# Optimization experiments

Hardware: AMD Instinct MI355X
Metric: run time of the kernel (lower is better)

## Reference

```python
import jax, jax.numpy as jnp
import numpy as np
import math

B, S, D = 4, 1024, 1024
NH, HD = 16, 64
I = 4096
EPS = 1e-12


def layer_norm(x, g, b):
    mu = jnp.mean(x, axis=-1, keepdims=True)
    var = jnp.mean((x - mu) ** 2, axis=-1, keepdims=True)
    return (x - mu) * jax.lax.rsqrt(var + EPS) * g + b


def setup_inputs() -> dict:
    key = jax.random.key(0)
    ks = jax.random.split(key, 12)
    s = 0.02
    return {
        "hidden_states": jax.random.normal(ks[0], (B, S, D), jnp.float32),
        "attention_mask": jnp.zeros((B, 1, 1, S), jnp.float32),
        "Wq": jax.random.normal(ks[1], (D, D), jnp.float32) * s,
        "bq": jnp.zeros((D,), jnp.float32),
        "Wk": jax.random.normal(ks[2], (D, D), jnp.float32) * s,
        "bk": jnp.zeros((D,), jnp.float32),
        "Wv": jax.random.normal(ks[3], (D, D), jnp.float32) * s,
        "bv": jnp.zeros((D,), jnp.float32),
        "Wo": jax.random.normal(ks[4], (D, D), jnp.float32) * s,
        "bo": jnp.zeros((D,), jnp.float32),
        "ln1_g": jnp.ones((D,), jnp.float32),
        "ln1_b": jnp.zeros((D,), jnp.float32),
        "Wi": jax.random.normal(ks[5], (D, I), jnp.float32) * s,
        "bi": jnp.zeros((I,), jnp.float32),
        "Wout": jax.random.normal(ks[6], (I, D), jnp.float32) * s,
        "bout": jnp.zeros((D,), jnp.float32),
        "ln2_g": jnp.ones((D,), jnp.float32),
        "ln2_b": jnp.zeros((D,), jnp.float32),
    }


def reference(hidden_states, attention_mask, Wq, bq, Wk, bk, Wv, bv, Wo, bo,
              ln1_g, ln1_b, Wi, bi, Wout, bout, ln2_g, ln2_b):
    h = hidden_states
    # QKV projections, split into heads: [B,S,D] -> [B,NH,S,HD]
    def heads(x):
        return x.reshape(B, S, NH, HD).transpose(0, 2, 1, 3)
    q = heads(h @ Wq + bq)
    k = heads(h @ Wk + bk)
    v = heads(h @ Wv + bv)
    # manual attention: scores [B,NH,S,S]
    scores = jnp.einsum("bhqd,bhkd->bhqk", q, k) / math.sqrt(HD)
    scores = scores + attention_mask
    probs = jax.nn.softmax(scores, axis=-1)
    ctx = jnp.einsum("bhqk,bhkd->bhqd", probs, v)
    ctx = ctx.transpose(0, 2, 1, 3).reshape(B, S, D)
    # self-output: dense + residual + LN
    attn_out = layer_norm(ctx @ Wo + bo + h, ln1_g, ln1_b)
    # FFN: dense + exact gelu, dense + residual + LN
    inter = jax.nn.gelu(attn_out @ Wi + bi, approximate=False)
    out = layer_norm(inter @ Wout + bout + attn_out, ln2_g, ln2_b)
    return out
```

## Files before the change

### kernel.cpp

```cpp
#include <hip/hip_runtime.h>
#include <hip/hip_bf16.h>
#include <math.h>

#define B_ 4
#define S_ 1024
#define D_ 1024
#define NH_ 16
#define HD_ 64
#define I_ 4096
#define M_ (B_*S_)

typedef __bf16 bf16_8 __attribute__((ext_vector_type(8)));
typedef float f32x4 __attribute__((ext_vector_type(4)));
typedef unsigned int u32x2 __attribute__((ext_vector_type(2)));
typedef unsigned short u16;

struct P4 { float* p[4]; };
struct T4 { const float* s[4]; u16* d[4]; };

__device__ __forceinline__ u16 f2b(float x) {
    __hip_bfloat16 h = __float2bfloat16(x);
    return *reinterpret_cast<u16*>(&h);
}

__device__ __forceinline__ void gload16(const void* g, void* l) {
    __builtin_amdgcn_global_load_lds(
        (const __attribute__((address_space(1))) void*)g,
        (__attribute__((address_space(3))) void*)l, 16, 0, 0);
}

__global__ __launch_bounds__(256) void cvt_bf16(
    const float4* __restrict__ in, ushort4* __restrict__ out, int n4)
{
    int i = blockIdx.x * 256 + threadIdx.x;
    if (i < n4) {
        float4 v = in[i];
        ushort4 o;
        o.x = f2b(v.x); o.y = f2b(v.y); o.z = f2b(v.z); o.w = f2b(v.w);
        out[i] = o;
    }
}

__global__ __launch_bounds__(256) void transpose_cvt(
    const float* __restrict__ in, u16* __restrict__ out, int K, int N)
{
    __shared__ float t[32][33];
    const int tid = threadIdx.x;
    const int k0 = blockIdx.y * 32, n0 = blockIdx.x * 32;
#pragma unroll
    for (int i = 0; i < 4; ++i) {
        int idx = i * 256 + tid;
        int r = idx >> 5, c = idx & 31;
        t[r][c] = in[(size_t)(k0 + r) * N + n0 + c];
    }
    __syncthreads();
    const int rr = tid >> 3, cc0 = (tid & 7) * 4;
    ushort4 o;
    o.x = f2b(t[cc0 + 0][rr]);
    o.y = f2b(t[cc0 + 1][rr]);
    o.z = f2b(t[cc0 + 2][rr]);
    o.w = f2b(t[cc0 + 3][rr]);
    *(ushort4*)(out + (size_t)(n0 + rr) * K + k0 + cc0) = o;
}

__global__ __launch_bounds__(256) void transpose4_cvt(T4 t4)
{
    __shared__ float t[32][33];
    const int tid = threadIdx.x;
    const int k0 = blockIdx.y * 32, n0 = blockIdx.x * 32;
    const float* in = t4.s[blockIdx.z];
    u16* out = t4.d[blockIdx.z];
#pragma unroll
    for (int i = 0; i < 4; ++i) {
        int idx = i * 256 + tid;
        int r = idx >> 5, c = idx & 31;
        t[r][c] = in[(size_t)(k0 + r) * D_ + n0 + c];
    }
    __syncthreads();
    const int rr = tid >> 3, cc0 = (tid & 7) * 4;
    ushort4 o;
    o.x = f2b(t[cc0 + 0][rr]);
    o.y = f2b(t[cc0 + 1][rr]);
    o.z = f2b(t[cc0 + 2][rr]);
    o.w = f2b(t[cc0 + 3][rr]);
    *(ushort4*)(out + (size_t)(n0 + rr) * D_ + k0 + cc0) = o;
}

#define NT_ 16

template<int MODE>
__global__ __launch_bounds__(512, 2) void gemm256(
    const u16* __restrict__ A, const u16* __restrict__ Bt,
    const float* __restrict__ b0, const float* __restrict__ b1,
    const float* __restrict__ b2,
    u16* __restrict__ outB, P4 parts, int N, int sA, int sB)
{
    __shared__ __align__(16) char sm[131072];

    const int tid  = threadIdx.x;
    const int lane = tid & 63, wid = tid >> 6;
    const int l15  = lane & 15, lg = lane >> 4;
    const int gm   = wid >> 2, gn = wid & 3;
    const int bm   = blockIdx.y * 256, bn = blockIdx.x * 256;
    const int koff = blockIdx.z * 1024;

    const int srow = (wid << 3) + (lane >> 3);
    const int skb  = ((lane & 7) << 4) ^ (((lane >> 3) & 7) << 4);
    const int scol = skb >> 1;
    const int xm   = (l15 & 7) << 4;

    f32x4 acc[8][4];
#pragma unroll
    for (int m = 0; m < 8; ++m)
#pragma unroll
        for (int j = 0; j < 4; ++j) {
            acc[m][j][0] = 0.f; acc[m][j][1] = 0.f;
            acc[m][j][2] = 0.f; acc[m][j][3] = 0.f;
        }

    auto stageA = [&](int v, int h) {
        const u16* src = A + (size_t)(bm + h * 128 + srow) * sA + koff + v * 64 + scol;
        char* dst = sm + ((v & 1) * 65536 + h * 16384 + wid * 1024);
        gload16(src, dst);
        gload16(src + (size_t)64 * sA, dst + 8192);
    };
    auto stageB = [&](int v, int h) {
        const u16* src = Bt + (size_t)(bn + h * 128 + srow) * sB + koff + v * 64 + scol;
        char* dst = sm + ((v & 1) * 65536 + 32768 + h * 16384 + wid * 1024);
        gload16(src, dst);
        gload16(src + (size_t)64 * sB, dst + 8192);
    };

    bf16_8 a[8], bb[2];
    auto loadA = [&](int vb, int s) {
        const char* base = sm + (vb * 65536 + gm * 16384);
#pragma unroll
        for (int m = 0; m < 8; ++m)
            a[m] = *(const bf16_8*)(base + (m * 16 + l15) * 128 +
                                    ((s * 64 + lg * 16) ^ xm));
    };
    auto loadB = [&](int vb, int s, int np) {
        const char* base = sm + (vb * 65536 + 32768 + (gn >> 1) * 16384);
#pragma unroll
        for (int j = 0; j < 2; ++j)
            bb[j] = *(const bf16_8*)(base + ((gn & 1) * 64 + (np * 2 + j) * 16 + l15) * 128 +
                                     ((s * 64 + lg * 16) ^ xm));
    };
    auto mfma16 = [&](int np) {
#pragma unroll
        for (int m = 0; m < 8; ++m)
#pragma unroll
            for (int j = 0; j < 2; ++j)
                acc[m][np * 2 + j] = __builtin_amdgcn_mfma_f32_16x16x32_bf16(
                    a[m], bb[j], acc[m][np * 2 + j], 0, 0, 0);
    };

    stageA(0, 0); stageA(0, 1);
    stageB(0, 0); stageB(0, 1);
    stageA(1, 0); stageA(1, 1);
    asm volatile("s_waitcnt vmcnt(4)" ::: "memory");
    __builtin_amdgcn_sched_barrier(0);
    __builtin_amdgcn_s_barrier();

    for (int v = 0; v < NT_ - 2; ++v) {
        const int vb = v & 1;
        loadA(vb, 0); loadB(vb, 0, 0);
        stageB(v + 1, 0); stageB(v + 1, 1);
        __builtin_amdgcn_s_barrier();
        asm volatile("s_waitcnt lgkmcnt(0)" ::: "memory");
        __builtin_amdgcn_s_setprio(1); mfma16(0); __builtin_amdgcn_s_setprio(0);
        __builtin_amdgcn_s_barrier();
        loadB(vb, 0, 1);
        __builtin_amdgcn_s_barrier();
        asm volatile("s_waitcnt lgkmcnt(0)" ::: "memory");
        __builtin_amdgcn_s_setprio(1); mfma16(1); __builtin_amdgcn_s_setprio(0);
        __builtin_amdgcn_s_barrier();
        loadA(vb, 1); loadB(vb, 1, 0);
        __builtin_amdgcn_s_barrier();
        asm volatile("s_waitcnt lgkmcnt(0)" ::: "memory");
        __builtin_amdgcn_s_setprio(1); mfma16(0); __builtin_amdgcn_s_setprio(0);
        __builtin_amdgcn_s_barrier();
        loadB(vb, 1, 1);
        stageA(v + 2, 0); stageA(v + 2, 1);
        __builtin_amdgcn_s_barrier();
        asm volatile("s_waitcnt lgkmcnt(0)" ::: "memory");
        __builtin_amdgcn_s_setprio(1); mfma16(1); __builtin_amdgcn_s_setprio(0);
        asm volatile("s_waitcnt vmcnt(4)" ::: "memory");
        __builtin_amdgcn_sched_barrier(0);
        __builtin_amdgcn_s_barrier();
    }
    {
        const int vb = (NT_ - 2) & 1;
        loadA(vb, 0); loadB(vb, 0, 0);
        stageB(NT_ - 1, 0); stageB(NT_ - 1, 1);
        __builtin_amdgcn_s_barrier();
        asm volatile("s_waitcnt lgkmcnt(0)" ::: "memory");
        __builtin_amdgcn_s_setprio(1); mfma16(0); __builtin_amdgcn_s_setprio(0);
        __builtin_amdgcn_s_barrier();
        loadB(vb, 0, 1);
        __builtin_amdgcn_s_barrier();
        asm volatile("s_waitcnt lgkmcnt(0)" ::: "memory");
        __builtin_amdgcn_s_setprio(1); mfma16(1); __builtin_amdgcn_s_setprio(0);
        __builtin_amdgcn_s_barrier();
        loadA(vb, 1); loadB(vb, 1, 0);
        __builtin_amdgcn_s_barrier();
        asm volatile("s_waitcnt lgkmcnt(0)" ::: "memory");
        __builtin_amdgcn_s_setprio(1); mfma16(0); __builtin_amdgcn_s_setprio(0);
        __builtin_amdgcn_s_barrier();
        loadB(vb, 1, 1);
        __builtin_amdgcn_s_barrier();
        asm volatile("s_waitcnt lgkmcnt(0)" ::: "memory");
        __builtin_amdgcn_s_setprio(1); mfma16(1); __builtin_amdgcn_s_setprio(0);
        asm volatile("s_waitcnt vmcnt(0)" ::: "memory");
        __builtin_amdgcn_sched_barrier(0);
        __builtin_amdgcn_s_barrier();
    }
    {
        const int vb = (NT_ - 1) & 1;
        loadA(vb, 0); loadB(vb, 0, 0); mfma16(0);
        loadB(vb, 0, 1);               mfma16(1);
        loadA(vb, 1); loadB(vb, 1, 0); mfma16(0);
        loadB(vb, 1, 1);               mfma16(1);
    }

    if (MODE == 2) {
        float* oP = parts.p[blockIdx.z];
#pragma unroll
        for (int m = 0; m < 8; ++m)
#pragma unroll
            for (int r = 0; r < 4; ++r) {
                const int row = bm + gm * 128 + m * 16 + lg * 4 + r;
#pragma unroll
                for (int j = 0; j < 4; ++j)
                    oP[(size_t)row * N + bn + gn * 64 + j * 16 + l15] = acc[m][j][r];
            }
    } else {
        const int cg = (bn + gn * 64) >> 10;
        const float* bp = (MODE == 0) ? (cg == 0 ? b0 : cg == 1 ? b1 : b2) : b0;
        const int cbase = (MODE == 0) ? ((bn + gn * 64) & 1023) : (bn + gn * 64);
        float bs[4];
#pragma unroll
        for (int j = 0; j < 4; ++j) bs[j] = bp[cbase + j * 16 + l15];
#pragma unroll
        for (int m = 0; m < 8; ++m)
#pragma unroll
            for (int r = 0; r < 4; ++r) {
                const int row = bm + gm * 128 + m * 16 + lg * 4 + r;
#pragma unroll
                for (int j = 0; j < 4; ++j) {
                    float v = acc[m][j][r] + bs[j];
                    if (MODE == 1) {
                        const float u = v * (1.5957691216f + 0.0713548163f * v * v);
                        v = __fdividef(v, 1.0f + __expf(-u));
                    }
                    outB[(size_t)row * N + bn + gn * 64 + j * 16 + l15] = f2b(v);
                }
            }
    }
}

__global__ __launch_bounds__(256) void gemm_splitk(
    const u16* __restrict__ A, const u16* __restrict__ Bt,
    P4 parts, int N, int K, int kchunk)
{
    __shared__ __align__(16) u16 As[128 * 32];
    __shared__ __align__(16) u16 Bs[128 * 32];

    const int tid  = threadIdx.x;
    const int lane = tid & 63, wid = tid >> 6;
    const int l15  = lane & 15, lg = lane >> 4;
    const int wm   = (wid >> 1) * 64, wn = (wid & 1) * 64;
    const int bm   = blockIdx.y * 128, bn = blockIdx.x * 128;
    const int wbase16 = (tid & ~63) * 16;
    const int kt0 = blockIdx.z * kchunk, kt1 = kt0 + kchunk;
    float* outP = parts.p[blockIdx.z];

    const int r0 = tid >> 2;
    const int c0 = (tid & 3) * 8;

    f32x4 acc[4][4];
#pragma unroll
    for (int i = 0; i < 4; ++i)
#pragma unroll
        for (int j = 0; j < 4; ++j) {
            acc[i][j][0] = 0.f; acc[i][j][1] = 0.f;
            acc[i][j][2] = 0.f; acc[i][j][3] = 0.f;
        }

    for (int kt = kt0; kt < kt1; kt += 32) {
        __syncthreads();
        gload16(A  + (size_t)(bm + r0)      * K + kt + c0, (char*)As + wbase16);
        gload16(A  + (size_t)(bm + r0 + 64) * K + kt + c0, (char*)As + wbase16 + 4096);
        gload16(Bt + (size_t)(bn + r0)      * K + kt + c0, (char*)Bs + wbase16);
        gload16(Bt + (size_t)(bn + r0 + 64) * K + kt + c0, (char*)Bs + wbase16 + 4096);
        __syncthreads();

        bf16_8 af[4], bfr[4];
#pragma unroll
        for (int f = 0; f < 4; ++f) {
            af[f]  = *(const bf16_8*)((const char*)As + (wm + f * 16 + l15) * 64 + lg * 16);
            bfr[f] = *(const bf16_8*)((const char*)Bs + (wn + f * 16 + l15) * 64 + lg * 16);
        }
#pragma unroll
        for (int i = 0; i < 4; ++i)
#pragma unroll
            for (int j = 0; j < 4; ++j)
                acc[i][j] = __builtin_amdgcn_mfma_f32_16x16x32_bf16(
                    af[i], bfr[j], acc[i][j], 0, 0, 0);
    }

#pragma unroll
    for (int i = 0; i < 4; ++i)
#pragma unroll
        for (int r = 0; r < 4; ++r) {
            const int row = bm + wm + i * 16 + lg * 4 + r;
#pragma unroll
            for (int j = 0; j < 4; ++j)
                outP[(size_t)row * N + bn + wn + j * 16 + l15] = acc[i][j][r];
        }
}

template<int NPART>
__global__ __launch_bounds__(256) void ln_reduce(
    P4 parts, const float* __restrict__ bias, const float* __restrict__ res,
    const float* __restrict__ g, const float* __restrict__ b,
    float* __restrict__ O, u16* __restrict__ OB)
{
    const int row = blockIdx.x;
    const int tid = threadIdx.x;
    const size_t off = (size_t)row * D_ + tid * 4;

    float4 v = *(const float4*)(res + off);
    const float4 bi = *(const float4*)(bias + tid * 4);
    v.x += bi.x; v.y += bi.y; v.z += bi.z; v.w += bi.w;
#pragma unroll
    for (int p = 0; p < NPART; ++p) {
        const float4 t = *(const float4*)(parts.p[p] + off);
        v.x += t.x; v.y += t.y; v.z += t.z; v.w += t.w;
    }

    float s  = v.x + v.y + v.z + v.w;
    float sq = v.x * v.x + v.y * v.y + v.z * v.z + v.w * v.w;
#pragma unroll
    for (int o = 32; o; o >>= 1) {
        s  += __shfl_down(s, o);
        sq += __shfl_down(sq, o);
    }
    __shared__ float red[8];
    const int wid = tid >> 6, lane = tid & 63;
    if (lane == 0) { red[wid] = s; red[4 + wid] = sq; }
    __syncthreads();
    const float ts = red[0] + red[1] + red[2] + red[3];
    const float tq = red[4] + red[5] + red[6] + red[7];
    const float mu  = ts * (1.0f / D_);
    const float var = tq * (1.0f / D_) - mu * mu;
    const float rs  = rsqrtf(var + 1e-12f);

    const float4 gv = *(const float4*)(g + tid * 4);
    const float4 bv = *(const float4*)(b + tid * 4);
    float4 o;
    o.x = (v.x - mu) * rs * gv.x + bv.x;
    o.y = (v.y - mu) * rs * gv.y + bv.y;
    o.z = (v.z - mu) * rs * gv.z + bv.z;
    o.w = (v.w - mu) * rs * gv.w + bv.w;
    *(float4*)(O + off) = o;
    if (OB) {
        ushort4 ob;
        ob.x = f2b(o.x); ob.y = f2b(o.y); ob.z = f2b(o.z); ob.w = f2b(o.w);
        *(ushort4*)(OB + off) = ob;
    }
}

__global__ __launch_bounds__(512) void attn_mfma(
    const u16* __restrict__ Qb, const u16* __restrict__ Kb,
    const u16* __restrict__ Vb, const float* __restrict__ mask,
    u16* __restrict__ ctxb, int qs)
{
    __shared__ __align__(16) char sm[32768];
    char* Ksm = sm;
    char* Vsm = sm + 8192;

    const int tid  = threadIdx.x;
    const int lane = tid & 63, wid = tid >> 6;
    char* Psm = sm + 16384 + wid * 2048;
    const int l15 = lane & 15, lg = lane >> 4;

    const int wg  = blockIdx.x;
    const int swz = (wg & 7) * 64 + (wg >> 3);
    const int b   = swz >> 7;
    const int h   = (swz >> 3) & 15;
    const int qb  = swz & 7;

    const int q0 = qb * 128 + wid * 16;
    const size_t inhead  = ((size_t)b * S_) * qs + (size_t)h * 64;
    const size_t outhead = ((size_t)b * S_) * D_ + (size_t)h * 64;

    const u16* Qrow = Qb + inhead + (size_t)(q0 + l15) * qs;
    const bf16_8 qf0 = *(const bf16_8*)(Qrow + lg * 8);
    const bf16_8 qf1 = *(const bf16_8*)(Qrow + 32 + lg * 8);

    f32x4 ctx[4];
#pragma unroll
    for (int i = 0; i < 4; ++i) { ctx[i][0]=0.f; ctx[i][1]=0.f; ctx[i][2]=0.f; ctx[i][3]=0.f; }
    float m_r = -1e30f, l_r = 0.f;

    const int skey = tid >> 3;
    const int sd0  = (tid & 7) * 8;
    const int xo_p = (l15 & 7) << 4;
    const int kwoff = skey * 128 + ((sd0 * 2) ^ ((skey & 7) << 4));
    const int vwoff = (sd0 >> 4) * 2048 + skey * 32 + ((sd0 & 8) << 1);

    const __attribute__((address_space(3))) char* vtr =
        (const __attribute__((address_space(3))) char*)(Vsm + lg * 256 + l15 * 2);

    bf16_8 kreg = *(const bf16_8*)(Kb + inhead + (size_t)skey * qs + sd0);
    bf16_8 vreg = *(const bf16_8*)(Vb + inhead + (size_t)skey * qs + sd0);

    for (int t = 0; t < S_ / 64; ++t) {
        __syncthreads();
        *(bf16_8*)(Ksm + kwoff) = kreg;
        *(bf16_8*)(Vsm + vwoff) = vreg;
        __syncthreads();
        if (t < S_ / 64 - 1) {
            const size_t noff = inhead + (size_t)((t + 1) * 64 + skey) * qs + sd0;
            kreg = *(const bf16_8*)(Kb + noff);
            vreg = *(const bf16_8*)(Vb + noff);
        }

        f32x4 sc[4];
#pragma unroll
        for (int kf = 0; kf < 4; ++kf) {
            const int key = kf * 16 + l15;
            f32x4 a; a[0]=0.f; a[1]=0.f; a[2]=0.f; a[3]=0.f;
            const bf16_8 kA = *(const bf16_8*)(Ksm + key * 128 + ((lg * 16)      ^ xo_p));
            a = __builtin_amdgcn_mfma_f32_16x16x32_bf16(kA, qf0, a, 0, 0, 0);
            const bf16_8 kB = *(const bf16_8*)(Ksm + key * 128 + ((64 + lg * 16) ^ xo_p));
            a = __builtin_amdgcn_mfma_f32_16x16x32_bf16(kB, qf1, a, 0, 0, 0);
            sc[kf] = a;
        }

        float p[16];
        float tmax = -1e30f;
#pragma unroll
        for (int kf = 0; kf < 4; ++kf) {
            const float4 mk = *(const float4*)(mask + (size_t)b * S_ + t * 64 + kf * 16 + lg * 4);
#pragma unroll
            for (int r = 0; r < 4; ++r) {
                const float mkr = (r == 0) ? mk.x : (r == 1) ? mk.y : (r == 2) ? mk.z : mk.w;
                p[kf * 4 + r] = sc[kf][r] * 0.125f + mkr;
                tmax = fmaxf(tmax, p[kf * 4 + r]);
            }
        }
        tmax = fmaxf(tmax, __shfl_xor(tmax, 16));
        tmax = fmaxf(tmax, __shfl_xor(tmax, 32));

        const float mnew = fmaxf(m_r, tmax);
        const float scl  = __expf(m_r - mnew);
        m_r = mnew;

        float psum = 0.f;
#pragma unroll
        for (int i = 0; i < 16; ++i) {
            p[i] = __expf(p[i] - mnew);
            psum += p[i];
        }
        psum += __shfl_xor(psum, 16);
        psum += __shfl_xor(psum, 32);
        l_r = l_r * scl + psum;

#pragma unroll
        for (int fd = 0; fd < 4; ++fd)
#pragma unroll
            for (int r = 0; r < 4; ++r) ctx[fd][r] *= scl;

#pragma unroll
        for (int kf = 0; kf < 4; ++kf)
#pragma unroll
            for (int rr = 0; rr < 2; ++rr) {
                ushort2 wv;
                wv.x = f2b(p[kf * 4 + 2 * rr]);
                wv.y = f2b(p[kf * 4 + 2 * rr + 1]);
                *(ushort2*)(Psm + l15 * 128 +
                            (((kf * 16 + lg * 4 + 2 * rr) * 2) ^ xo_p)) = wv;
            }
        asm volatile("s_waitcnt lgkmcnt(0)" ::: "memory");

#pragma unroll
        for (int s = 0; s < 2; ++s) {
            const bf16_8 pf = *(const bf16_8*)(Psm + l15 * 128 +
                                ((s * 64 + lg * 16) ^ xo_p));
            const __attribute__((address_space(3))) char* a3 = vtr + s * 1024;
            u32x2 r0, r1, r2, r3, r4, r5, r6, r7;
            asm volatile(
                "ds_read_b64_tr_b16 %0, %8 offset:0\n\t"
                "ds_read_b64_tr_b16 %1, %8 offset:128\n\t"
                "ds_read_b64_tr_b16 %2, %8 offset:2048\n\t"
                "ds_read_b64_tr_b16 %3, %8 offset:2176\n\t"
                "ds_read_b64_tr_b16 %4, %8 offset:4096\n\t"
                "ds_read_b64_tr_b16 %5, %8 offset:4224\n\t"
                "ds_read_b64_tr_b16 %6, %8 offset:6144\n\t"
                "ds_read_b64_tr_b16 %7, %8 offset:6272\n\t"
                "s_waitcnt lgkmcnt(0)"
                : "=&v"(r0), "=&v"(r1), "=&v"(r2), "=&v"(r3),
                  "=&v"(r4), "=&v"(r5), "=&v"(r6), "=&v"(r7)
                : "v"(a3));
            union Cv { unsigned u[4]; bf16_8 v; };
            Cv c0; c0.u[0] = r0.x; c0.u[1] = r0.y; c0.u[2] = r1.x; c0.u[3] = r1.y;
            Cv c1; c1.u[0] = r2.x; c1.u[1] = r2.y; c1.u[2] = r3.x; c1.u[3] = r3.y;
            Cv c2; c2.u[0] = r4.x; c2.u[1] = r4.y; c2.u[2] = r5.x; c2.u[3] = r5.y;
            Cv c3; c3.u[0] = r6.x; c3.u[1] = r6.y; c3.u[2] = r7.x; c3.u[3] = r7.y;
            ctx[0] = __builtin_amdgcn_mfma_f32_16x16x32_bf16(c0.v, pf, ctx[0], 0, 0, 0);
            ctx[1] = __builtin_amdgcn_mfma_f32_16x16x32_bf16(c1.v, pf, ctx[1], 0, 0, 0);
            ctx[2] = __builtin_amdgcn_mfma_f32_16x16x32_bf16(c2.v, pf, ctx[2], 0, 0, 0);
            ctx[3] = __builtin_amdgcn_mfma_f32_16x16x32_bf16(c3.v, pf, ctx[3], 0, 0, 0);
        }
    }

    const float inv = 1.f / l_r;
    const size_t qrow = outhead + (size_t)(q0 + l15) * D_;
#pragma unroll
    for (int fd = 0; fd < 4; ++fd) {
        ushort4 o;
        o.x = f2b(ctx[fd][0] * inv);
        o.y = f2b(ctx[fd][1] * inv);
        o.z = f2b(ctx[fd][2] * inv);
        o.w = f2b(ctx[fd][3] * inv);
        *(ushort4*)(ctxb + qrow + fd * 16 + lg * 4) = o;
    }
}

extern "C" void kernel_launch(void* const* d_in, const int* in_sizes, int n_in,
                              void* d_out, int out_size, void* d_ws, size_t ws_size,
                              hipStream_t stream)
{
    const float* h    = (const float*)d_in[0];
    const float* mask = (const float*)d_in[1];
    const float* Wq   = (const float*)d_in[2];
    const float* bq   = (const float*)d_in[3];
    const float* Wk   = (const float*)d_in[4];
    const float* bk   = (const float*)d_in[5];
    const float* Wv   = (const float*)d_in[6];
    const float* bv   = (const float*)d_in[7];
    const float* Wo   = (const float*)d_in[8];
    const float* bo   = (const float*)d_in[9];
    const float* ln1g = (const float*)d_in[10];
    const float* ln1b = (const float*)d_in[11];
    const float* Wi   = (const float*)d_in[12];
    const float* bi   = (const float*)d_in[13];
    const float* Wout = (const float*)d_in[14];
    const float* bout = (const float*)d_in[15];
    const float* ln2g = (const float*)d_in[16];
    const float* ln2b = (const float*)d_in[17];
    float* out = (float*)d_out;

    char* w = (char*)d_ws;
    const size_t MiB = 1ull << 20;
    u16*   Woutt  = (u16*)(w + 0);
    float* attnF  = (float*)(w + 8 * MiB);
    float* woP0   = attnF;
    float* woP1   = (float*)(w + 24 * MiB);
    u16*   interB = (u16*)(w + 24 * MiB);
    u16*   hb     = (u16*)(w + 56 * MiB);
    float* ffP0   = (float*)(w + 56 * MiB);
    u16*   Wqkvt  = (u16*)(w + 64 * MiB);
    u16*   Wot    = (u16*)(w + 70 * MiB);
    float* ffP1   = (float*)(w + 72 * MiB);
    u16*   Wit    = (u16*)(w + 72 * MiB);
    float* ffP2   = (float*)(w + 88 * MiB);
    u16*   QKVb   = (u16*)(w + 80 * MiB);
    u16*   ctxb   = (u16*)(w + 104 * MiB);
    float* ffP3   = (float*)(w + 104 * MiB);
    u16*   attnB  = (u16*)(w + 112 * MiB);

    const dim3 blk(256);
    P4 zp; zp.p[0] = zp.p[1] = zp.p[2] = zp.p[3] = nullptr;

    cvt_bf16<<<dim3((M_ * D_ / 4) / 256), blk, 0, stream>>>(
        (const float4*)h, (ushort4*)hb, M_ * D_ / 4);
    T4 t4;
    t4.s[0] = Wq; t4.s[1] = Wk; t4.s[2] = Wv; t4.s[3] = Wo;
    t4.d[0] = Wqkvt; t4.d[1] = Wqkvt + 1024 * 1024;
    t4.d[2] = Wqkvt + 2 * 1024 * 1024; t4.d[3] = Wot;
    transpose4_cvt<<<dim3(32, 32, 4), blk, 0, stream>>>(t4);
    transpose_cvt<<<dim3(128, 32), blk, 0, stream>>>(Wi,   Wit,   D_, I_);
    transpose_cvt<<<dim3(32, 128), blk, 0, stream>>>(Wout, Woutt, I_, D_);

    gemm256<0><<<dim3(12, 16, 1), dim3(512), 0, stream>>>(
        hb, Wqkvt, bq, bk, bv, QKVb, zp, 3072, 1024, 1024);

    attn_mfma<<<dim3(512), dim3(512), 0, stream>>>(
        QKVb, QKVb + 1024, QKVb + 2048, mask, ctxb, 3072);

    P4 woP; woP.p[0] = woP0; woP.p[1] = woP1; woP.p[2] = nullptr; woP.p[3] = nullptr;
    gemm_splitk<<<dim3(8, 32, 2), blk, 0, stream>>>(ctxb, Wot, woP, D_, D_, 512);
    ln_reduce<2><<<dim3(M_), blk, 0, stream>>>(woP, bo, h, ln1g, ln1b, attnF, attnB);

    gemm256<1><<<dim3(16, 16, 1), dim3(512), 0, stream>>>(
        attnB, Wit, bi, nullptr, nullptr, interB, zp, 4096, 1024, 1024);

    P4 ffP; ffP.p[0] = ffP0; ffP.p[1] = ffP1; ffP.p[2] = ffP2; ffP.p[3] = ffP3;
    gemm256<2><<<dim3(4, 16, 4), dim3(512), 0, stream>>>(
        interB, Woutt, nullptr, nullptr, nullptr, nullptr, ffP, 1024, 4096, 4096);
    ln_reduce<4><<<dim3(M_), blk, 0, stream>>>(ffP, bout, attnF, ln2g, ln2b, out, nullptr);
}
```

Before: 219.3 us.

## Store split-K partials in bf16 and template GEMM strides as constants

Split-K partial sums from the Wo and Wout GEMMs are now written and read as bf16 instead of fp32, halving their write and re-read traffic in ln_reduce. The workspace layout is reshuffled to fit the smaller buffers. GEMM strides and N become template constants so address math can fold at compile time. The GELU epilogue is switched from a tanh/sigmoid approximation to an erf polynomial, which is closer to exact GELU but costs more arithmetic. Rounding partials to bf16 before summation adds precision loss.

```diff
diff --git a/kernel.cpp b/kernel.cpp
--- a/kernel.cpp
+++ b/kernel.cpp
@@ -15,18 +15,32 @@
 typedef unsigned int u32x2 __attribute__((ext_vector_type(2)));
 typedef unsigned short u16;
 
-struct P4 { float* p[4]; };
+struct PB { u16* p[4]; };
 struct T4 { const float* s[4]; u16* d[4]; };
 
 __device__ __forceinline__ u16 f2b(float x) {
     __hip_bfloat16 h = __float2bfloat16(x);
     return *reinterpret_cast<u16*>(&h);
+}
+__device__ __forceinline__ float b2f(u16 x) {
+    return __uint_as_float(((unsigned)x) << 16);
 }
 
 __device__ __forceinline__ void gload16(const void* g, void* l) {
     __builtin_amdgcn_global_load_lds(
         (const __attribute__((address_space(1))) void*)g,
         (__attribute__((address_space(3))) void*)l, 16, 0, 0);
+}
+
+__device__ __forceinline__ float gelu_f(float v) {
+    const float z  = v * 0.70710678118654752f;
+    const float az = fabsf(z);
+    const float t  = __fdividef(1.0f, 1.0f + 0.3275911f * az);
+    const float poly = t * (0.254829592f + t * (-0.284496736f +
+                       t * (1.421413741f + t * (-1.453152027f + t * 1.061405429f))));
+    const float erfa = 1.0f - poly * __expf(-z * z);
+    const float erfv = copysignf(erfa, z);
+    return 0.5f * v * (1.0f + erfv);
 }
 
 __global__ __launch_bounds__(256) void cvt_bf16(
@@ -88,12 +102,12 @@
 
 #define NT_ 16
 
-template<int MODE>
+template<int MODE, int SA, int SB, int NN>
 __global__ __launch_bounds__(512, 2) void gemm256(
     const u16* __restrict__ A, const u16* __restrict__ Bt,
     const float* __restrict__ b0, const float* __restrict__ b1,
     const float* __restrict__ b2,
-    u16* __restrict__ outB, P4 parts, int N, int sA, int sB)
+    u16* __restrict__ outB, PB parts)
 {
     __shared__ __align__(16) char sm[131072];
 
@@ -102,7 +116,7 @@
     const int l15  = lane & 15, lg = lane >> 4;
     const int gm   = wid >> 2, gn = wid & 3;
     const int bm   = blockIdx.y * 256, bn = blockIdx.x * 256;
-    const int koff = blockIdx.z * 1024;
+    const int koff = (MODE == 2) ? blockIdx.z * 1024 : 0;
 
     const int srow = (wid << 3) + (lane >> 3);
     const int skb  = ((lane & 7) << 4) ^ (((lane >> 3) & 7) << 4);
@@ -119,16 +133,16 @@
         }
 
     auto stageA = [&](int v, int h) {
-        const u16* src = A + (size_t)(bm + h * 128 + srow) * sA + koff + v * 64 + scol;
+        const u16* src = A + (size_t)(bm + h * 128 + srow) * SA + koff + v * 64 + scol;
         char* dst = sm + ((v & 1) * 65536 + h * 16384 + wid * 1024);
         gload16(src, dst);
-        gload16(src + (size_t)64 * sA, dst + 8192);
+        gload16(src + (size_t)64 * SA, dst + 8192);
     };
     auto stageB = [&](int v, int h) {
-        const u16* src = Bt + (size_t)(bn + h * 128 + srow) * sB + koff + v * 64 + scol;
+        const u16* src = Bt + (size_t)(bn + h * 128 + srow) * SB + koff + v * 64 + scol;
         char* dst = sm + ((v & 1) * 65536 + 32768 + h * 16384 + wid * 1024);
         gload16(src, dst);
-        gload16(src + (size_t)64 * sB, dst + 8192);
+        gload16(src + (size_t)64 * SB, dst + 8192);
     };
 
     bf16_8 a[8], bb[2];
@@ -224,7 +238,7 @@
     }
 
     if (MODE == 2) {
-        float* oP = parts.p[blockIdx.z];
+        u16* oP = parts.p[blockIdx.z];
 #pragma unroll
         for (int m = 0; m < 8; ++m)
 #pragma unroll
@@ -232,7 +246,7 @@
                 const int row = bm + gm * 128 + m * 16 + lg * 4 + r;
 #pragma unroll
                 for (int j = 0; j < 4; ++j)
-                    oP[(size_t)row * N + bn + gn * 64 + j * 16 + l15] = acc[m][j][r];
+                    oP[(size_t)row * NN + bn + gn * 64 + j * 16 + l15] = f2b(acc[m][j][r]);
             }
     } else {
         const int cg = (bn + gn * 64) >> 10;
@@ -249,11 +263,8 @@
 #pragma unroll
                 for (int j = 0; j < 4; ++j) {
                     float v = acc[m][j][r] + bs[j];
-                    if (MODE == 1) {
-                        const float u = v * (1.5957691216f + 0.0713548163f * v * v);
-                        v = __fdividef(v, 1.0f + __expf(-u));
-                    }
-                    outB[(size_t)row * N + bn + gn * 64 + j * 16 + l15] = f2b(v);
+                    if (MODE == 1) v = gelu_f(v);
+                    outB[(size_t)row * NN + bn + gn * 64 + j * 16 + l15] = f2b(v);
                 }
             }
     }
@@ -261,7 +272,7 @@
 
 __global__ __launch_bounds__(256) void gemm_splitk(
     const u16* __restrict__ A, const u16* __restrict__ Bt,
-    P4 parts, int N, int K, int kchunk)
+    PB parts, int N, int K, int kchunk)
 {
     __shared__ __align__(16) u16 As[128 * 32];
     __shared__ __align__(16) u16 Bs[128 * 32];
@@ -273,7 +284,7 @@
     const int bm   = blockIdx.y * 128, bn = blockIdx.x * 128;
     const int wbase16 = (tid & ~63) * 16;
     const int kt0 = blockIdx.z * kchunk, kt1 = kt0 + kchunk;
-    float* outP = parts.p[blockIdx.z];
+    u16* outP = parts.p[blockIdx.z];
 
     const int r0 = tid >> 2;
     const int c0 = (tid & 3) * 8;
@@ -316,13 +327,13 @@
             const int row = bm + wm + i * 16 + lg * 4 + r;
 #pragma unroll
             for (int j = 0; j < 4; ++j)
-                outP[(size_t)row * N + bn + wn + j * 16 + l15] = acc[i][j][r];
+                outP[(size_t)row * N + bn + wn + j * 16 + l15] = f2b(acc[i][j][r]);
         }
 }
 
 template<int NPART>
 __global__ __launch_bounds__(256) void ln_reduce(
-    P4 parts, const float* __restrict__ bias, const float* __restrict__ res,
+    PB parts, const float* __restrict__ bias, const float* __restrict__ res,
     const float* __restrict__ g, const float* __restrict__ b,
     float* __restrict__ O, u16* __restrict__ OB)
 {
@@ -335,8 +346,8 @@
     v.x += bi.x; v.y += bi.y; v.z += bi.z; v.w += bi.w;
 #pragma unroll
     for (int p = 0; p < NPART; ++p) {
-        const float4 t = *(const float4*)(parts.p[p] + off);
-        v.x += t.x; v.y += t.y; v.z += t.z; v.w += t.w;
+        const ushort4 t = *(const ushort4*)(parts.p[p] + off);
+        v.x += b2f(t.x); v.y += b2f(t.y); v.z += b2f(t.z); v.w += b2f(t.w);
     }
 
     float s  = v.x + v.y + v.z + v.w;
@@ -556,24 +567,24 @@
     char* w = (char*)d_ws;
     const size_t MiB = 1ull << 20;
     u16*   Woutt  = (u16*)(w + 0);
-    float* attnF  = (float*)(w + 8 * MiB);
-    float* woP0   = attnF;
-    float* woP1   = (float*)(w + 24 * MiB);
-    u16*   interB = (u16*)(w + 24 * MiB);
-    u16*   hb     = (u16*)(w + 56 * MiB);
-    float* ffP0   = (float*)(w + 56 * MiB);
-    u16*   Wqkvt  = (u16*)(w + 64 * MiB);
-    u16*   Wot    = (u16*)(w + 70 * MiB);
-    float* ffP1   = (float*)(w + 72 * MiB);
-    u16*   Wit    = (u16*)(w + 72 * MiB);
-    float* ffP2   = (float*)(w + 88 * MiB);
-    u16*   QKVb   = (u16*)(w + 80 * MiB);
-    u16*   ctxb   = (u16*)(w + 104 * MiB);
-    float* ffP3   = (float*)(w + 104 * MiB);
-    u16*   attnB  = (u16*)(w + 112 * MiB);
+    u16*   Wit    = (u16*)(w + 8 * MiB);
+    u16*   hb     = (u16*)(w + 16 * MiB);
+    u16*   woP0   = (u16*)(w + 16 * MiB);
+    u16*   ffP1   = (u16*)(w + 16 * MiB);
+    u16*   Wqkvt  = (u16*)(w + 24 * MiB);
+    u16*   ffP2   = (u16*)(w + 24 * MiB);
+    u16*   Wot    = (u16*)(w + 30 * MiB);
+    u16*   QKVb   = (u16*)(w + 32 * MiB);
+    u16*   woP1   = (u16*)(w + 32 * MiB);
+    u16*   ffP3   = (u16*)(w + 32 * MiB);
+    float* attnF  = (float*)(w + 40 * MiB);
+    u16*   attnB  = (u16*)(w + 56 * MiB);
+    u16*   interB = (u16*)(w + 64 * MiB);
+    u16*   ctxb   = (u16*)(w + 96 * MiB);
+    u16*   ffP0   = (u16*)(w + 96 * MiB);
 
     const dim3 blk(256);
-    P4 zp; zp.p[0] = zp.p[1] = zp.p[2] = zp.p[3] = nullptr;
+    PB zp; zp.p[0] = zp.p[1] = zp.p[2] = zp.p[3] = nullptr;
 
     cvt_bf16<<<dim3((M_ * D_ / 4) / 256), blk, 0, stream>>>(
         (const float4*)h, (ushort4*)hb, M_ * D_ / 4);
@@ -585,21 +596,21 @@
     transpose_cvt<<<dim3(128, 32), blk, 0, stream>>>(Wi,   Wit,   D_, I_);
     transpose_cvt<<<dim3(32, 128), blk, 0, stream>>>(Wout, Woutt, I_, D_);
 
-    gemm256<0><<<dim3(12, 16, 1), dim3(512), 0, stream>>>(
-        hb, Wqkvt, bq, bk, bv, QKVb, zp, 3072, 1024, 1024);
+    gemm256<0, 1024, 1024, 3072><<<dim3(12, 16, 1), dim3(512), 0, stream>>>(
+        hb, Wqkvt, bq, bk, bv, QKVb, zp);
 
     attn_mfma<<<dim3(512), dim3(512), 0, stream>>>(
         QKVb, QKVb + 1024, QKVb + 2048, mask, ctxb, 3072);
 
-    P4 woP; woP.p[0] = woP0; woP.p[1] = woP1; woP.p[2] = nullptr; woP.p[3] = nullptr;
+    PB woP; woP.p[0] = woP0; woP.p[1] = woP1; woP.p[2] = nullptr; woP.p[3] = nullptr;
     gemm_splitk<<<dim3(8, 32, 2), blk, 0, stream>>>(ctxb, Wot, woP, D_, D_, 512);
     ln_reduce<2><<<dim3(M_), blk, 0, stream>>>(woP, bo, h, ln1g, ln1b, attnF, attnB);
 
-    gemm256<1><<<dim3(16, 16, 1), dim3(512), 0, stream>>>(
-        attnB, Wit, bi, nullptr, nullptr, interB, zp, 4096, 1024, 1024);
-
-    P4 ffP; ffP.p[0] = ffP0; ffP.p[1] = ffP1; ffP.p[2] = ffP2; ffP.p[3] = ffP3;
-    gemm256<2><<<dim3(4, 16, 4), dim3(512), 0, stream>>>(
-        interB, Woutt, nullptr, nullptr, nullptr, nullptr, ffP, 1024, 4096, 4096);
+    gemm256<1, 1024, 1024, 4096><<<dim3(16, 16, 1), dim3(512), 0, stream>>>(
+        attnB, Wit, bi, nullptr, nullptr, interB, zp);
+
+    PB ffP; ffP.p[0] = ffP0; ffP.p[1] = ffP1; ffP.p[2] = ffP2; ffP.p[3] = ffP3;
+    gemm256<2, 4096, 4096, 1024><<<dim3(4, 16, 4), dim3(512), 0, stream>>>(
+        interB, Woutt, nullptr, nullptr, nullptr, nullptr, ffP);
     ln_reduce<4><<<dim3(M_), blk, 0, stream>>>(ffP, bout, attnF, ln2g, ln2b, out, nullptr);
 }
```

Measured after the change: 213.7 us. -2.5%, faster.
